# Kernel optimization log

Measured on AMD Instinct MI355X. Metric: run time of the kernel, lower is better.

The kernel has to match this reference:

```python
import jax, jax.numpy as jnp
import numpy as np

DIM = 512
NUM_HEADS = 16
HEAD_DIM = DIM // NUM_HEADS
SCALE = HEAD_DIM ** -0.5  # qk_scale default


def setup_inputs() -> dict:
    key = jax.random.key(0)
    k1, k2, k3 = jax.random.split(key, 3)
    B, nH, nW, C = 8, 256, 49, DIM
    x = jax.random.normal(k1, (B, nH, nW, C), dtype=jnp.float32)
    x_all = jax.random.normal(k2, (B, nH, nW, C), dtype=jnp.float32)
    W_qkv = jax.random.normal(k3, (C, 3 * C), dtype=jnp.float32) * (C ** -0.5)
    b_qkv = jnp.zeros((3 * C,), dtype=jnp.float32)
    return {"x": x, "x_all": x_all, "W_qkv": W_qkv, "b_qkv": b_qkv}


def reference(x, x_all, W_qkv, b_qkv):
    # x: [B, nH, nW, C]  (nH = num windows, nW = tokens per window)
    B, nH, nW, C = x.shape
    qkv = x @ W_qkv + b_qkv                      # [B, nH, nW, 3C]
    qkv = qkv.reshape(B, nH, nW, 3, C)
    q, k, v = qkv[..., 0, :], qkv[..., 1, :], qkv[..., 2, :]
    q = q * SCALE
    attn = jnp.einsum("bwic,bwjc->bwij", q, k)   # [B, nH, nW, nW]
    attn = jax.nn.softmax(attn, axis=-1)
    out = jnp.einsum("bwij,bwjc->bwic", attn, v)  # [B, nH, nW, C]
    return out
```

## Files before the change

kernel.cpp:

```cpp
#include <hip/hip_runtime.h>

typedef __bf16 bf16;
typedef __bf16 bf16x4 __attribute__((ext_vector_type(4)));
typedef __bf16 bf16x8 __attribute__((ext_vector_type(8)));
typedef float f32x16 __attribute__((ext_vector_type(16)));

#define SCALE 0.17677669529663687f

__device__ inline f32x16 fzero16() {
  f32x16 v;
  #pragma unroll
  for (int i = 0; i < 16; ++i) v[i] = 0.f;
  return v;
}

__global__ __launch_bounds__(256) void k_mqk(const float* __restrict__ W, bf16* __restrict__ Mqk) {
  __shared__ float Wkt[32][65];
  __shared__ float Wqt[32][65];
  const int tb = (blockIdx.x >> 4) * 32;
  const int ta = (blockIdx.x & 15) * 32;
  const int tid = threadIdx.x;
  const int a_l = tid & 31, b_l = (tid >> 5) * 4;
  float acc[4] = {0.f, 0.f, 0.f, 0.f};
  for (int c0 = 0; c0 < 512; c0 += 64) {
    __syncthreads();
    for (int i = tid; i < 2048; i += 256) {
      int r = i >> 6, c = i & 63;
      Wkt[r][c] = W[(size_t)(tb + r) * 1536 + 512 + c0 + c];
      Wqt[r][c] = W[(size_t)(ta + r) * 1536 + c0 + c];
    }
    __syncthreads();
    for (int c = 0; c < 64; ++c) {
      float wq = Wqt[a_l][c];
      #pragma unroll
      for (int i = 0; i < 4; ++i) acc[i] += Wkt[b_l + i][c] * wq;
    }
  }
  #pragma unroll
  for (int i = 0; i < 4; ++i)
    Mqk[(size_t)(tb + b_l + i) * 512 + ta + a_l] = (bf16)(SCALE * acc[i]);
}

__global__ __launch_bounds__(256) void k_wvt(const float* __restrict__ W, bf16* __restrict__ WvT) {
  const int cin = blockIdx.x;
  int n = threadIdx.x;
  WvT[(size_t)n * 512 + cin] = (bf16)W[(size_t)cin * 1536 + 1024 + n];
  n += 256;
  WvT[(size_t)n * 512 + cin] = (bf16)W[(size_t)cin * 1536 + 1024 + n];
}

__global__ __launch_bounds__(256) void k_w2(const float* __restrict__ W, const float* __restrict__ bqkv,
                                            float* __restrict__ w2) {
  __shared__ float red[256];
  const int b = blockIdx.x, tid = threadIdx.x;
  float s = W[(size_t)b * 1536 + 512 + tid] * bqkv[tid]
          + W[(size_t)b * 1536 + 512 + 256 + tid] * bqkv[256 + tid];
  red[tid] = s;
  __syncthreads();
  for (int ofs = 128; ofs > 0; ofs >>= 1) {
    if (tid < ofs) red[tid] += red[tid + ofs];
    __syncthreads();
  }
  if (tid == 0) w2[b] = SCALE * red[0];
}

struct SMem {
  bf16 Xs[64][520];
  union { bf16 T1s[64][520]; bf16 Vt[512][72]; } u;
  float Ss[52][65];
  bf16 Ps[64][72];
  float sbias[64];
};

__global__ __launch_bounds__(512, 2) void k_attn(
    const float* __restrict__ x, const float* __restrict__ bqkv,
    const bf16* __restrict__ Mqk, const bf16* __restrict__ WvT,
    const float* __restrict__ w2, float* __restrict__ out) {
  __shared__ SMem sm;
  const int tid = threadIdx.x;
  const int wave = tid >> 6, lane = tid & 63;
  const int lm = lane & 31, hk = lane >> 5;
  const int wid = blockIdx.x;
  const float* xw = x + (size_t)wid * 25088;

  for (int idx = tid; idx < 6272; idx += 512) {
    float4 f = ((const float4*)xw)[idx];
    int row = idx >> 7, c4 = (idx & 127) << 2;
    bf16x4 p;
    p[0] = (bf16)f.x; p[1] = (bf16)f.y; p[2] = (bf16)f.z; p[3] = (bf16)f.w;
    *(bf16x4*)&sm.Xs[row][c4] = p;
  }
  for (int idx = tid; idx < 15 * 130; idx += 512) {
    int r = 49 + idx / 130, c = (idx % 130) * 4;
    bf16x4 z; z[0] = (bf16)0.f; z[1] = (bf16)0.f; z[2] = (bf16)0.f; z[3] = (bf16)0.f;
    *(bf16x4*)&sm.Xs[r][c] = z;
  }
  __syncthreads();

  {
    const int n_base = wave * 64;
    f32x16 a00 = fzero16(), a01 = fzero16(), a10 = fzero16(), a11 = fzero16();
    const bf16* a0p = &sm.Xs[lm][0];
    const bf16* a1p = &sm.Xs[32 + lm][0];
    const bf16* b0g = Mqk + (size_t)(n_base + lm) * 512;
    const bf16* b1g = Mqk + (size_t)(n_base + 32 + lm) * 512;
    #pragma unroll 4
    for (int k0 = 0; k0 < 512; k0 += 16) {
      const int ko = k0 + 8 * hk;
      bf16x8 fa0 = *(const bf16x8*)(a0p + ko);
      bf16x8 fa1 = *(const bf16x8*)(a1p + ko);
      bf16x8 fb0 = *(const bf16x8*)(b0g + ko);
      bf16x8 fb1 = *(const bf16x8*)(b1g + ko);
      a00 = __builtin_amdgcn_mfma_f32_32x32x16_bf16(fa0, fb0, a00, 0, 0, 0);
      a01 = __builtin_amdgcn_mfma_f32_32x32x16_bf16(fa0, fb1, a01, 0, 0, 0);
      a10 = __builtin_amdgcn_mfma_f32_32x32x16_bf16(fa1, fb0, a10, 0, 0, 0);
      a11 = __builtin_amdgcn_mfma_f32_32x32x16_bf16(fa1, fb1, a11, 0, 0, 0);
    }
    #pragma unroll
    for (int reg = 0; reg < 16; ++reg) {
      const int row = (reg & 3) + 8 * (reg >> 2) + 4 * hk;
      sm.u.T1s[row][n_base + lm]           = (bf16)a00[reg];
      sm.u.T1s[row][n_base + 32 + lm]      = (bf16)a01[reg];
      sm.u.T1s[32 + row][n_base + lm]      = (bf16)a10[reg];
      sm.u.T1s[32 + row][n_base + 32 + lm] = (bf16)a11[reg];
    }
  }
  __syncthreads();

  if (wave < 4) {
    const int r = wave & 1, c = wave >> 1;
    f32x16 accS = fzero16();
    const bf16* ap = &sm.u.T1s[32 * r + lm][0];
    const bf16* bp = &sm.Xs[32 * c + lm][0];
    #pragma unroll 4
    for (int k0 = 0; k0 < 512; k0 += 16) {
      const int ko = k0 + 8 * hk;
      bf16x8 fa = *(const bf16x8*)(ap + ko);
      bf16x8 fb = *(const bf16x8*)(bp + ko);
      accS = __builtin_amdgcn_mfma_f32_32x32x16_bf16(fa, fb, accS, 0, 0, 0);
    }
    #pragma unroll
    for (int reg = 0; reg < 16; ++reg) {
      const int row = 32 * r + (reg & 3) + 8 * (reg >> 2) + 4 * hk;
      if (row < 52) sm.Ss[row][32 * c + lm] = accS[reg];
    }
  } else {
    const int t2 = tid - 256;
    const int j = t2 >> 2, part = t2 & 3;
    float s = 0.f;
    for (int cc = part * 128; cc < part * 128 + 128; ++cc)
      s += (float)sm.Xs[j][cc] * w2[cc];
    s += __shfl_xor(s, 1);
    s += __shfl_xor(s, 2);
    if (part == 0) sm.sbias[j] = s;
  }
  __syncthreads();

  if (tid < 49) {
    const int i = tid;
    float m = -1e30f;
    for (int j = 0; j < 49; ++j) m = fmaxf(m, sm.Ss[i][j] + sm.sbias[j]);
    float ssum = 0.f;
    for (int j = 0; j < 49; ++j) ssum += __expf(sm.Ss[i][j] + sm.sbias[j] - m);
    const float inv = 1.f / ssum;
    for (int j = 0; j < 49; ++j)
      sm.Ps[i][j] = (bf16)(__expf(sm.Ss[i][j] + sm.sbias[j] - m) * inv);
    for (int j = 49; j < 64; ++j) sm.Ps[i][j] = (bf16)0.f;
  }

  {
    const int n_base = wave * 64;
    f32x16 a00 = fzero16(), a01 = fzero16(), a10 = fzero16(), a11 = fzero16();
    const bf16* a0p = &sm.Xs[lm][0];
    const bf16* a1p = &sm.Xs[32 + lm][0];
    const bf16* b0g = WvT + (size_t)(n_base + lm) * 512;
    const bf16* b1g = WvT + (size_t)(n_base + 32 + lm) * 512;
    #pragma unroll 4
    for (int k0 = 0; k0 < 512; k0 += 16) {
      const int ko = k0 + 8 * hk;
      bf16x8 fa0 = *(const bf16x8*)(a0p + ko);
      bf16x8 fa1 = *(const bf16x8*)(a1p + ko);
      bf16x8 fb0 = *(const bf16x8*)(b0g + ko);
      bf16x8 fb1 = *(const bf16x8*)(b1g + ko);
      a00 = __builtin_amdgcn_mfma_f32_32x32x16_bf16(fa0, fb0, a00, 0, 0, 0);
      a01 = __builtin_amdgcn_mfma_f32_32x32x16_bf16(fa0, fb1, a01, 0, 0, 0);
      a10 = __builtin_amdgcn_mfma_f32_32x32x16_bf16(fa1, fb0, a10, 0, 0, 0);
      a11 = __builtin_amdgcn_mfma_f32_32x32x16_bf16(fa1, fb1, a11, 0, 0, 0);
    }
    const float bv0 = bqkv[1024 + n_base + lm];
    const float bv1 = bqkv[1024 + n_base + 32 + lm];
    #pragma unroll
    for (int g = 0; g < 4; ++g) {
      const int t0 = 8 * g + 4 * hk;
      bf16x4 p0, p1, p2, p3;
      #pragma unroll
      for (int j = 0; j < 4; ++j) {
        p0[j] = (bf16)(a00[4 * g + j] + bv0);
        p1[j] = (bf16)(a01[4 * g + j] + bv1);
        p2[j] = (bf16)(a10[4 * g + j] + bv0);
        p3[j] = (bf16)(a11[4 * g + j] + bv1);
      }
      *(bf16x4*)&sm.u.Vt[n_base + lm][t0]           = p0;
      *(bf16x4*)&sm.u.Vt[n_base + 32 + lm][t0]      = p1;
      *(bf16x4*)&sm.u.Vt[n_base + lm][32 + t0]      = p2;
      *(bf16x4*)&sm.u.Vt[n_base + 32 + lm][32 + t0] = p3;
    }
  }
  __syncthreads();

  {
    const int n_base = wave * 64;
    f32x16 a00 = fzero16(), a01 = fzero16(), a10 = fzero16(), a11 = fzero16();
    #pragma unroll
    for (int k0 = 0; k0 < 64; k0 += 16) {
      const int ko = k0 + 8 * hk;
      bf16x8 fa0 = *(const bf16x8*)&sm.Ps[lm][ko];
      bf16x8 fa1 = *(const bf16x8*)&sm.Ps[32 + lm][ko];
      bf16x8 fb0 = *(const bf16x8*)&sm.u.Vt[n_base + lm][ko];
      bf16x8 fb1 = *(const bf16x8*)&sm.u.Vt[n_base + 32 + lm][ko];
      a00 = __builtin_amdgcn_mfma_f32_32x32x16_bf16(fa0, fb0, a00, 0, 0, 0);
      a01 = __builtin_amdgcn_mfma_f32_32x32x16_bf16(fa0, fb1, a01, 0, 0, 0);
      a10 = __builtin_amdgcn_mfma_f32_32x32x16_bf16(fa1, fb0, a10, 0, 0, 0);
      a11 = __builtin_amdgcn_mfma_f32_32x32x16_bf16(fa1, fb1, a11, 0, 0, 0);
    }
    float* ow = out + (size_t)wid * 25088;
    const int c0_ = n_base + lm, c1_ = n_base + 32 + lm;
    #pragma unroll
    for (int reg = 0; reg < 16; ++reg) {
      const int row = (reg & 3) + 8 * (reg >> 2) + 4 * hk;
      if (row < 49) {
        ow[row * 512 + c0_] = a00[reg];
        ow[row * 512 + c1_] = a01[reg];
      }
      const int row1 = 32 + row;
      if (row1 < 49) {
        ow[row1 * 512 + c0_] = a10[reg];
        ow[row1 * 512 + c1_] = a11[reg];
      }
    }
  }
}

extern "C" void kernel_launch(void* const* d_in, const int* in_sizes, int n_in,
                              void* d_out, int out_size, void* d_ws, size_t ws_size,
                              hipStream_t stream) {
  const float* x    = (const float*)d_in[0];
  const float* W    = (const float*)d_in[2];
  const float* bqkv = (const float*)d_in[3];
  float* out = (float*)d_out;

  bf16*  Mqk = (bf16*)d_ws;
  bf16*  WvT = (bf16*)((char*)d_ws + 512 * 512 * 2);
  float* w2  = (float*)((char*)d_ws + 2 * 512 * 512 * 2);

  k_mqk<<<256, 256, 0, stream>>>(W, Mqk);
  k_wvt<<<512, 256, 0, stream>>>(W, WvT);
  k_w2 <<<512, 256, 0, stream>>>(W, bqkv, w2);
  k_attn<<<2048, 512, 0, stream>>>(x, bqkv, Mqk, WvT, w2, out);
}
```

Measured before the change: 768.7 us.

## Keep attention intermediates in registers, shrink LDS, raise occupancy to four blocks

Computes T1 transposed (Mqk·X^T) so each wave's accumulators can be repacked into MFMA operand fragments with cross-lane shuffles. QK scores are then accumulated across waves into LDS with atomicAdd, and V stays in registers for the PV product. This removes the T1s/Vt LDS buffers, padding-row zeroing and several barriers, which shrinks LDS enough to allow launch_bounds(512,4). The cost is extra register pressure, LDS atomics on the score matrix, and duplicated row-48 loads for the padded tail.

```diff
diff --git a/kernel.cpp b/kernel.cpp
--- a/kernel.cpp
+++ b/kernel.cpp
@@ -1,17 +1,45 @@
 #include <hip/hip_runtime.h>
+#include <stdint.h>
 
 typedef __bf16 bf16;
+typedef __bf16 bf16x2 __attribute__((ext_vector_type(2)));
 typedef __bf16 bf16x4 __attribute__((ext_vector_type(4)));
 typedef __bf16 bf16x8 __attribute__((ext_vector_type(8)));
 typedef float f32x16 __attribute__((ext_vector_type(16)));
 
 #define SCALE 0.17677669529663687f
-
-__device__ inline f32x16 fzero16() {
+#define MFMA32(a, b, c) __builtin_amdgcn_mfma_f32_32x32x16_bf16((a), (b), (c), 0, 0, 0)
+
+__device__ __forceinline__ f32x16 fzero16() {
   f32x16 v;
   #pragma unroll
   for (int i = 0; i < 16; ++i) v[i] = 0.f;
   return v;
+}
+
+__device__ __forceinline__ uint32_t pk2(float a, float b) {
+  union { bf16x2 h; uint32_t u; } c;
+  c.h[0] = (bf16)a; c.h[1] = (bf16)b;
+  return c.u;
+}
+
+template<int HALF>
+__device__ __forceinline__ bf16x8 repack_frag(f32x16 cc, int hk) {
+  const int R = 8 * HALF;
+  uint32_t pA0 = pk2(cc[R + 0], cc[R + 1]);
+  uint32_t pA1 = pk2(cc[R + 2], cc[R + 3]);
+  uint32_t pB0 = pk2(cc[R + 4], cc[R + 5]);
+  uint32_t pB1 = pk2(cc[R + 6], cc[R + 7]);
+  uint32_t sA0 = __shfl_xor(pA0, 32, 64);
+  uint32_t sA1 = __shfl_xor(pA1, 32, 64);
+  uint32_t sB0 = __shfl_xor(pB0, 32, 64);
+  uint32_t sB1 = __shfl_xor(pB1, 32, 64);
+  union { uint32_t u[4]; bf16x8 v; } o;
+  o.u[0] = hk ? sB0 : pA0;
+  o.u[1] = hk ? sB1 : pA1;
+  o.u[2] = hk ? pB0 : sA0;
+  o.u[3] = hk ? pB1 : sA1;
+  return o.v;
 }
 
 __global__ __launch_bounds__(256) void k_mqk(const float* __restrict__ W, bf16* __restrict__ Mqk) {
@@ -64,22 +92,24 @@
   if (tid == 0) w2[b] = SCALE * red[0];
 }
 
-struct SMem {
-  bf16 Xs[64][520];
-  union { bf16 T1s[64][520]; bf16 Vt[512][72]; } u;
-  float Ss[52][65];
-  bf16 Ps[64][72];
+struct __align__(16) SMem {
+  bf16  Xs[49][520];
+  bf16  Ps[64][72];
+  float Ss[49][65];
+  float ws2[512];
   float sbias[64];
 };
 
-__global__ __launch_bounds__(512, 2) void k_attn(
+__global__ __launch_bounds__(512, 4) void k_attn(
     const float* __restrict__ x, const float* __restrict__ bqkv,
     const bf16* __restrict__ Mqk, const bf16* __restrict__ WvT,
     const float* __restrict__ w2, float* __restrict__ out) {
   __shared__ SMem sm;
   const int tid = threadIdx.x;
-  const int wave = tid >> 6, lane = tid & 63;
+  const int lane = tid & 63;
   const int lm = lane & 31, hk = lane >> 5;
+  const int wave = tid >> 6;
+  const int n_base = wave * 64;
   const int wid = blockIdx.x;
   const float* xw = x + (size_t)wid * 25088;
 
@@ -90,153 +120,197 @@
     p[0] = (bf16)f.x; p[1] = (bf16)f.y; p[2] = (bf16)f.z; p[3] = (bf16)f.w;
     *(bf16x4*)&sm.Xs[row][c4] = p;
   }
-  for (int idx = tid; idx < 15 * 130; idx += 512) {
-    int r = 49 + idx / 130, c = (idx % 130) * 4;
-    bf16x4 z; z[0] = (bf16)0.f; z[1] = (bf16)0.f; z[2] = (bf16)0.f; z[3] = (bf16)0.f;
-    *(bf16x4*)&sm.Xs[r][c] = z;
-  }
+  sm.ws2[tid] = w2[tid];
+  for (int i = tid; i < 49 * 65; i += 512) ((float*)&sm.Ss[0][0])[i] = 0.f;
   __syncthreads();
 
-  {
-    const int n_base = wave * 64;
-    f32x16 a00 = fzero16(), a01 = fzero16(), a10 = fzero16(), a11 = fzero16();
-    const bf16* a0p = &sm.Xs[lm][0];
-    const bf16* a1p = &sm.Xs[32 + lm][0];
-    const bf16* b0g = Mqk + (size_t)(n_base + lm) * 512;
-    const bf16* b1g = Mqk + (size_t)(n_base + 32 + lm) * 512;
+  const bf16* xs_lo = &sm.Xs[lm][0];
+  const bf16* xs_hi = &sm.Xs[(32 + lm) < 49 ? (32 + lm) : 48][0];
+
+  f32x16 c100 = fzero16(), c101 = fzero16(), c110 = fzero16(), c111 = fzero16();
+  {
+    const bf16* mq0 = Mqk + (size_t)(n_base + lm) * 512;
+    const bf16* mq1 = Mqk + (size_t)(n_base + 32 + lm) * 512;
     #pragma unroll 4
     for (int k0 = 0; k0 < 512; k0 += 16) {
       const int ko = k0 + 8 * hk;
-      bf16x8 fa0 = *(const bf16x8*)(a0p + ko);
-      bf16x8 fa1 = *(const bf16x8*)(a1p + ko);
-      bf16x8 fb0 = *(const bf16x8*)(b0g + ko);
-      bf16x8 fb1 = *(const bf16x8*)(b1g + ko);
-      a00 = __builtin_amdgcn_mfma_f32_32x32x16_bf16(fa0, fb0, a00, 0, 0, 0);
-      a01 = __builtin_amdgcn_mfma_f32_32x32x16_bf16(fa0, fb1, a01, 0, 0, 0);
-      a10 = __builtin_amdgcn_mfma_f32_32x32x16_bf16(fa1, fb0, a10, 0, 0, 0);
-      a11 = __builtin_amdgcn_mfma_f32_32x32x16_bf16(fa1, fb1, a11, 0, 0, 0);
+      bf16x8 fa0 = *(const bf16x8*)(mq0 + ko);
+      bf16x8 fa1 = *(const bf16x8*)(mq1 + ko);
+      bf16x8 fb0 = *(const bf16x8*)(xs_lo + ko);
+      bf16x8 fb1 = *(const bf16x8*)(xs_hi + ko);
+      c100 = MFMA32(fa0, fb0, c100); c101 = MFMA32(fa0, fb1, c101);
+      c110 = MFMA32(fa1, fb0, c110); c111 = MFMA32(fa1, fb1, c111);
+    }
+  }
+
+  bf16x8 aT0s0 = repack_frag<0>(c100, hk);
+  bf16x8 aT0s1 = repack_frag<1>(c100, hk);
+  bf16x8 aT0s2 = repack_frag<0>(c110, hk);
+  bf16x8 aT0s3 = repack_frag<1>(c110, hk);
+  bf16x8 aT1s0 = repack_frag<0>(c101, hk);
+  bf16x8 aT1s1 = repack_frag<1>(c101, hk);
+  bf16x8 aT1s2 = repack_frag<0>(c111, hk);
+  bf16x8 aT1s3 = repack_frag<1>(c111, hk);
+
+  {
+    f32x16 s00 = fzero16(), s01 = fzero16(), s10 = fzero16(), s11 = fzero16();
+    const bf16* xb0 = xs_lo + n_base;
+    const bf16* xb1 = xs_hi + n_base;
+    const int ho = 8 * hk;
+    {
+      bf16x8 fb0 = *(const bf16x8*)(xb0 + ho +  0);
+      bf16x8 fb1 = *(const bf16x8*)(xb1 + ho +  0);
+      s00 = MFMA32(aT0s0, fb0, s00); s01 = MFMA32(aT0s0, fb1, s01);
+      s10 = MFMA32(aT1s0, fb0, s10); s11 = MFMA32(aT1s0, fb1, s11);
+    }
+    {
+      bf16x8 fb0 = *(const bf16x8*)(xb0 + ho + 16);
+      bf16x8 fb1 = *(const bf16x8*)(xb1 + ho + 16);
+      s00 = MFMA32(aT0s1, fb0, s00); s01 = MFMA32(aT0s1, fb1, s01);
+      s10 = MFMA32(aT1s1, fb0, s10); s11 = MFMA32(aT1s1, fb1, s11);
+    }
+    {
+      bf16x8 fb0 = *(const bf16x8*)(xb0 + ho + 32);
+      bf16x8 fb1 = *(const bf16x8*)(xb1 + ho + 32);
+      s00 = MFMA32(aT0s2, fb0, s00); s01 = MFMA32(aT0s2, fb1, s01);
+      s10 = MFMA32(aT1s2, fb0, s10); s11 = MFMA32(aT1s2, fb1, s11);
+    }
+    {
+      bf16x8 fb0 = *(const bf16x8*)(xb0 + ho + 48);
+      bf16x8 fb1 = *(const bf16x8*)(xb1 + ho + 48);
+      s00 = MFMA32(aT0s3, fb0, s00); s01 = MFMA32(aT0s3, fb1, s01);
+      s10 = MFMA32(aT1s3, fb0, s10); s11 = MFMA32(aT1s3, fb1, s11);
     }
     #pragma unroll
-    for (int reg = 0; reg < 16; ++reg) {
-      const int row = (reg & 3) + 8 * (reg >> 2) + 4 * hk;
-      sm.u.T1s[row][n_base + lm]           = (bf16)a00[reg];
-      sm.u.T1s[row][n_base + 32 + lm]      = (bf16)a01[reg];
-      sm.u.T1s[32 + row][n_base + lm]      = (bf16)a10[reg];
-      sm.u.T1s[32 + row][n_base + 32 + lm] = (bf16)a11[reg];
-    }
-  }
-  __syncthreads();
-
-  if (wave < 4) {
-    const int r = wave & 1, c = wave >> 1;
-    f32x16 accS = fzero16();
-    const bf16* ap = &sm.u.T1s[32 * r + lm][0];
-    const bf16* bp = &sm.Xs[32 * c + lm][0];
+    for (int r = 0; r < 16; ++r) {
+      const int row = (r & 3) + 8 * (r >> 2) + 4 * hk;
+      if (row < 49) {
+        atomicAdd(&sm.Ss[row][lm],      s00[r]);
+        atomicAdd(&sm.Ss[row][32 + lm], s01[r]);
+      }
+      const int row1 = 32 + row;
+      if (row1 < 49) {
+        atomicAdd(&sm.Ss[row1][lm],      s10[r]);
+        atomicAdd(&sm.Ss[row1][32 + lm], s11[r]);
+      }
+    }
+  }
+
+  {
+    const int brow = tid >> 3, bsub = tid & 7;
+    if (brow < 49) {
+      const bf16* xr = &sm.Xs[brow][bsub * 64];
+      const float* wr = &sm.ws2[bsub * 64];
+      float s = 0.f;
+      #pragma unroll
+      for (int t = 0; t < 8; ++t) {
+        bf16x8 xv = *(const bf16x8*)(xr + 8 * t);
+        #pragma unroll
+        for (int e = 0; e < 8; ++e) s += (float)xv[e] * wr[8 * t + e];
+      }
+      s += __shfl_xor(s, 1, 64);
+      s += __shfl_xor(s, 2, 64);
+      s += __shfl_xor(s, 4, 64);
+      if (bsub == 0) sm.sbias[brow] = s;
+    }
+  }
+
+  f32x16 v00 = fzero16(), v01 = fzero16(), v10 = fzero16(), v11 = fzero16();
+  {
+    const bf16* wv0 = WvT + (size_t)(n_base + lm) * 512;
+    const bf16* wv1 = WvT + (size_t)(n_base + 32 + lm) * 512;
     #pragma unroll 4
     for (int k0 = 0; k0 < 512; k0 += 16) {
       const int ko = k0 + 8 * hk;
-      bf16x8 fa = *(const bf16x8*)(ap + ko);
-      bf16x8 fb = *(const bf16x8*)(bp + ko);
-      accS = __builtin_amdgcn_mfma_f32_32x32x16_bf16(fa, fb, accS, 0, 0, 0);
-    }
-    #pragma unroll
-    for (int reg = 0; reg < 16; ++reg) {
-      const int row = 32 * r + (reg & 3) + 8 * (reg >> 2) + 4 * hk;
-      if (row < 52) sm.Ss[row][32 * c + lm] = accS[reg];
-    }
-  } else {
-    const int t2 = tid - 256;
-    const int j = t2 >> 2, part = t2 & 3;
-    float s = 0.f;
-    for (int cc = part * 128; cc < part * 128 + 128; ++cc)
-      s += (float)sm.Xs[j][cc] * w2[cc];
-    s += __shfl_xor(s, 1);
-    s += __shfl_xor(s, 2);
-    if (part == 0) sm.sbias[j] = s;
-  }
-  __syncthreads();
-
-  if (tid < 49) {
-    const int i = tid;
-    float m = -1e30f;
-    for (int j = 0; j < 49; ++j) m = fmaxf(m, sm.Ss[i][j] + sm.sbias[j]);
-    float ssum = 0.f;
-    for (int j = 0; j < 49; ++j) ssum += __expf(sm.Ss[i][j] + sm.sbias[j] - m);
-    const float inv = 1.f / ssum;
-    for (int j = 0; j < 49; ++j)
-      sm.Ps[i][j] = (bf16)(__expf(sm.Ss[i][j] + sm.sbias[j] - m) * inv);
-    for (int j = 49; j < 64; ++j) sm.Ps[i][j] = (bf16)0.f;
-  }
-
-  {
-    const int n_base = wave * 64;
-    f32x16 a00 = fzero16(), a01 = fzero16(), a10 = fzero16(), a11 = fzero16();
-    const bf16* a0p = &sm.Xs[lm][0];
-    const bf16* a1p = &sm.Xs[32 + lm][0];
-    const bf16* b0g = WvT + (size_t)(n_base + lm) * 512;
-    const bf16* b1g = WvT + (size_t)(n_base + 32 + lm) * 512;
-    #pragma unroll 4
-    for (int k0 = 0; k0 < 512; k0 += 16) {
-      const int ko = k0 + 8 * hk;
-      bf16x8 fa0 = *(const bf16x8*)(a0p + ko);
-      bf16x8 fa1 = *(const bf16x8*)(a1p + ko);
-      bf16x8 fb0 = *(const bf16x8*)(b0g + ko);
-      bf16x8 fb1 = *(const bf16x8*)(b1g + ko);
-      a00 = __builtin_amdgcn_mfma_f32_32x32x16_bf16(fa0, fb0, a00, 0, 0, 0);
-      a01 = __builtin_amdgcn_mfma_f32_32x32x16_bf16(fa0, fb1, a01, 0, 0, 0);
-      a10 = __builtin_amdgcn_mfma_f32_32x32x16_bf16(fa1, fb0, a10, 0, 0, 0);
-      a11 = __builtin_amdgcn_mfma_f32_32x32x16_bf16(fa1, fb1, a11, 0, 0, 0);
+      bf16x8 fa0 = *(const bf16x8*)(xs_lo + ko);
+      bf16x8 fa1 = *(const bf16x8*)(xs_hi + ko);
+      bf16x8 fb0 = *(const bf16x8*)(wv0 + ko);
+      bf16x8 fb1 = *(const bf16x8*)(wv1 + ko);
+      v00 = MFMA32(fa0, fb0, v00); v01 = MFMA32(fa0, fb1, v01);
+      v10 = MFMA32(fa1, fb0, v10); v11 = MFMA32(fa1, fb1, v11);
     }
     const float bv0 = bqkv[1024 + n_base + lm];
     const float bv1 = bqkv[1024 + n_base + 32 + lm];
     #pragma unroll
-    for (int g = 0; g < 4; ++g) {
-      const int t0 = 8 * g + 4 * hk;
-      bf16x4 p0, p1, p2, p3;
-      #pragma unroll
-      for (int j = 0; j < 4; ++j) {
-        p0[j] = (bf16)(a00[4 * g + j] + bv0);
-        p1[j] = (bf16)(a01[4 * g + j] + bv1);
-        p2[j] = (bf16)(a10[4 * g + j] + bv0);
-        p3[j] = (bf16)(a11[4 * g + j] + bv1);
-      }
-      *(bf16x4*)&sm.u.Vt[n_base + lm][t0]           = p0;
-      *(bf16x4*)&sm.u.Vt[n_base + 32 + lm][t0]      = p1;
-      *(bf16x4*)&sm.u.Vt[n_base + lm][32 + t0]      = p2;
-      *(bf16x4*)&sm.u.Vt[n_base + 32 + lm][32 + t0] = p3;
-    }
-  }
+    for (int r = 0; r < 16; ++r) {
+      v00[r] += bv0; v01[r] += bv1; v10[r] += bv0; v11[r] += bv1;
+    }
+  }
+  bf16x8 bV00 = repack_frag<0>(v00, hk);
+  bf16x8 bV01 = repack_frag<1>(v00, hk);
+  bf16x8 bV02 = repack_frag<0>(v10, hk);
+  bf16x8 bV03 = repack_frag<1>(v10, hk);
+  bf16x8 bV10 = repack_frag<0>(v01, hk);
+  bf16x8 bV11 = repack_frag<1>(v01, hk);
+  bf16x8 bV12 = repack_frag<0>(v11, hk);
+  bf16x8 bV13 = repack_frag<1>(v11, hk);
+
   __syncthreads();
 
   {
-    const int n_base = wave * 64;
-    f32x16 a00 = fzero16(), a01 = fzero16(), a10 = fzero16(), a11 = fzero16();
-    #pragma unroll
-    for (int k0 = 0; k0 < 64; k0 += 16) {
-      const int ko = k0 + 8 * hk;
-      bf16x8 fa0 = *(const bf16x8*)&sm.Ps[lm][ko];
-      bf16x8 fa1 = *(const bf16x8*)&sm.Ps[32 + lm][ko];
-      bf16x8 fb0 = *(const bf16x8*)&sm.u.Vt[n_base + lm][ko];
-      bf16x8 fb1 = *(const bf16x8*)&sm.u.Vt[n_base + 32 + lm][ko];
-      a00 = __builtin_amdgcn_mfma_f32_32x32x16_bf16(fa0, fb0, a00, 0, 0, 0);
-      a01 = __builtin_amdgcn_mfma_f32_32x32x16_bf16(fa0, fb1, a01, 0, 0, 0);
-      a10 = __builtin_amdgcn_mfma_f32_32x32x16_bf16(fa1, fb0, a10, 0, 0, 0);
-      a11 = __builtin_amdgcn_mfma_f32_32x32x16_bf16(fa1, fb1, a11, 0, 0, 0);
-    }
-    float* ow = out + (size_t)wid * 25088;
-    const int c0_ = n_base + lm, c1_ = n_base + 32 + lm;
-    #pragma unroll
-    for (int reg = 0; reg < 16; ++reg) {
-      const int row = (reg & 3) + 8 * (reg >> 2) + 4 * hk;
-      if (row < 49) {
-        ow[row * 512 + c0_] = a00[reg];
-        ow[row * 512 + c1_] = a01[reg];
-      }
-      const int row1 = 32 + row;
-      if (row1 < 49) {
-        ow[row1 * 512 + c0_] = a10[reg];
-        ow[row1 * 512 + c1_] = a11[reg];
-      }
+    const int srow = tid >> 3, sub = tid & 7;
+    if (srow < 49) {
+      float v[8];
+      #pragma unroll
+      for (int t = 0; t < 8; ++t) {
+        const int col = sub + 8 * t;
+        v[t] = (col < 49) ? (sm.Ss[srow][col] + sm.sbias[col]) : -1e30f;
+      }
+      float m = v[0];
+      #pragma unroll
+      for (int t = 1; t < 8; ++t) m = fmaxf(m, v[t]);
+      m = fmaxf(m, __shfl_xor(m, 1, 64));
+      m = fmaxf(m, __shfl_xor(m, 2, 64));
+      m = fmaxf(m, __shfl_xor(m, 4, 64));
+      float e[8]; float ssum = 0.f;
+      #pragma unroll
+      for (int t = 0; t < 8; ++t) {
+        const int col = sub + 8 * t;
+        e[t] = (col < 49) ? __expf(v[t] - m) : 0.f;
+        ssum += e[t];
+      }
+      ssum += __shfl_xor(ssum, 1, 64);
+      ssum += __shfl_xor(ssum, 2, 64);
+      ssum += __shfl_xor(ssum, 4, 64);
+      const float inv = 1.f / ssum;
+      #pragma unroll
+      for (int t = 0; t < 8; ++t)
+        sm.Ps[srow][sub + 8 * t] = (bf16)(e[t] * inv);
+    }
+  }
+  __syncthreads();
+
+  f32x16 o00 = fzero16(), o01 = fzero16(), o10 = fzero16(), o11 = fzero16();
+  {
+    const bf16* p0 = &sm.Ps[lm][8 * hk];
+    const bf16* p1 = &sm.Ps[32 + lm][8 * hk];
+    bf16x8 fa0, fa1;
+    fa0 = *(const bf16x8*)(p0 +  0); fa1 = *(const bf16x8*)(p1 +  0);
+    o00 = MFMA32(fa0, bV00, o00); o01 = MFMA32(fa0, bV10, o01);
+    o10 = MFMA32(fa1, bV00, o10); o11 = MFMA32(fa1, bV10, o11);
+    fa0 = *(const bf16x8*)(p0 + 16); fa1 = *(const bf16x8*)(p1 + 16);
+    o00 = MFMA32(fa0, bV01, o00); o01 = MFMA32(fa0, bV11, o01);
+    o10 = MFMA32(fa1, bV01, o10); o11 = MFMA32(fa1, bV11, o11);
+    fa0 = *(const bf16x8*)(p0 + 32); fa1 = *(const bf16x8*)(p1 + 32);
+    o00 = MFMA32(fa0, bV02, o00); o01 = MFMA32(fa0, bV12, o01);
+    o10 = MFMA32(fa1, bV02, o10); o11 = MFMA32(fa1, bV12, o11);
+    fa0 = *(const bf16x8*)(p0 + 48); fa1 = *(const bf16x8*)(p1 + 48);
+    o00 = MFMA32(fa0, bV03, o00); o01 = MFMA32(fa0, bV13, o01);
+    o10 = MFMA32(fa1, bV03, o10); o11 = MFMA32(fa1, bV13, o11);
+  }
+  float* ow = out + (size_t)wid * 25088;
+  const int c0_ = n_base + lm, c1_ = n_base + 32 + lm;
+  #pragma unroll
+  for (int r = 0; r < 16; ++r) {
+    const int row = (r & 3) + 8 * (r >> 2) + 4 * hk;
+    if (row < 49) {
+      ow[row * 512 + c0_] = o00[r];
+      ow[row * 512 + c1_] = o01[r];
+    }
+    const int row1 = 32 + row;
+    if (row1 < 49) {
+      ow[row1 * 512 + c0_] = o10[r];
+      ow[row1 * 512 + c1_] = o11[r];
     }
   }
 }
```

New measurement: 916.9 us. 19.3% more time.

## Fuse V projection into first GEMM loop, parallelize softmax, tile WvT transpose

Applied to the files above, without the earlier changes.

The V projection GEMM is merged into the X·Mqk loop, so each loaded X fragment feeds eight MFMAs and the X shared-memory reads are shared. The V accumulators stay in registers across the score and softmax phases. Softmax now uses 8 threads per row with shuffle reductions instead of one serial thread per row. The WvT transpose kernel now goes through a shared-memory tile with coalesced vector accesses. Holding 128 extra accumulator registers through the middle phases may raise register pressure or cause spills and lower occupancy.

```diff
diff --git a/kernel.cpp b/kernel.cpp
--- a/kernel.cpp
+++ b/kernel.cpp
@@ -1,4 +1,5 @@
 #include <hip/hip_runtime.h>
+#include <stdint.h>
 
 typedef __bf16 bf16;
 typedef __bf16 bf16x4 __attribute__((ext_vector_type(4)));
@@ -6,8 +7,9 @@
 typedef float f32x16 __attribute__((ext_vector_type(16)));
 
 #define SCALE 0.17677669529663687f
-
-__device__ inline f32x16 fzero16() {
+#define MFMA32(a, b, c) __builtin_amdgcn_mfma_f32_32x32x16_bf16((a), (b), (c), 0, 0, 0)
+
+__device__ __forceinline__ f32x16 fzero16() {
   f32x16 v;
   #pragma unroll
   for (int i = 0; i < 16; ++i) v[i] = 0.f;
@@ -42,11 +44,32 @@
 }
 
 __global__ __launch_bounds__(256) void k_wvt(const float* __restrict__ W, bf16* __restrict__ WvT) {
-  const int cin = blockIdx.x;
-  int n = threadIdx.x;
-  WvT[(size_t)n * 512 + cin] = (bf16)W[(size_t)cin * 1536 + 1024 + n];
-  n += 256;
-  WvT[(size_t)n * 512 + cin] = (bf16)W[(size_t)cin * 1536 + 1024 + n];
+  __shared__ float Wt[64][68];
+  const int cin0  = (blockIdx.x & 7) * 64;
+  const int cout0 = (blockIdx.x >> 3) * 64;
+  const int tid = threadIdx.x;
+  {
+    const int r = tid >> 2, cq = (tid & 3) * 16;
+    #pragma unroll
+    for (int cc = 0; cc < 4; ++cc) {
+      float4 f = *(const float4*)&W[(size_t)(cin0 + r) * 1536 + 1024 + cout0 + cq + 4 * cc];
+      Wt[r][cq + 4 * cc + 0] = f.x;
+      Wt[r][cq + 4 * cc + 1] = f.y;
+      Wt[r][cq + 4 * cc + 2] = f.z;
+      Wt[r][cq + 4 * cc + 3] = f.w;
+    }
+  }
+  __syncthreads();
+  {
+    const int co = tid >> 2, seg = (tid & 3) * 16;
+    bf16x8 p0, p1;
+    #pragma unroll
+    for (int e = 0; e < 8; ++e) p0[e] = (bf16)Wt[seg + e][co];
+    #pragma unroll
+    for (int e = 0; e < 8; ++e) p1[e] = (bf16)Wt[seg + 8 + e][co];
+    *(bf16x8*)&WvT[(size_t)(cout0 + co) * 512 + cin0 + seg]     = p0;
+    *(bf16x8*)&WvT[(size_t)(cout0 + co) * 512 + cin0 + seg + 8] = p1;
+  }
 }
 
 __global__ __launch_bounds__(256) void k_w2(const float* __restrict__ W, const float* __restrict__ bqkv,
@@ -97,32 +120,38 @@
   }
   __syncthreads();
 
+  f32x16 v00, v01, v10, v11;
   {
     const int n_base = wave * 64;
-    f32x16 a00 = fzero16(), a01 = fzero16(), a10 = fzero16(), a11 = fzero16();
+    f32x16 t00 = fzero16(), t01 = fzero16(), t10 = fzero16(), t11 = fzero16();
+    v00 = fzero16(); v01 = fzero16(); v10 = fzero16(); v11 = fzero16();
     const bf16* a0p = &sm.Xs[lm][0];
     const bf16* a1p = &sm.Xs[32 + lm][0];
     const bf16* b0g = Mqk + (size_t)(n_base + lm) * 512;
     const bf16* b1g = Mqk + (size_t)(n_base + 32 + lm) * 512;
-    #pragma unroll 4
+    const bf16* c0g = WvT + (size_t)(n_base + lm) * 512;
+    const bf16* c1g = WvT + (size_t)(n_base + 32 + lm) * 512;
+    #pragma unroll 2
     for (int k0 = 0; k0 < 512; k0 += 16) {
       const int ko = k0 + 8 * hk;
       bf16x8 fa0 = *(const bf16x8*)(a0p + ko);
       bf16x8 fa1 = *(const bf16x8*)(a1p + ko);
       bf16x8 fb0 = *(const bf16x8*)(b0g + ko);
       bf16x8 fb1 = *(const bf16x8*)(b1g + ko);
-      a00 = __builtin_amdgcn_mfma_f32_32x32x16_bf16(fa0, fb0, a00, 0, 0, 0);
-      a01 = __builtin_amdgcn_mfma_f32_32x32x16_bf16(fa0, fb1, a01, 0, 0, 0);
-      a10 = __builtin_amdgcn_mfma_f32_32x32x16_bf16(fa1, fb0, a10, 0, 0, 0);
-      a11 = __builtin_amdgcn_mfma_f32_32x32x16_bf16(fa1, fb1, a11, 0, 0, 0);
+      bf16x8 fc0 = *(const bf16x8*)(c0g + ko);
+      bf16x8 fc1 = *(const bf16x8*)(c1g + ko);
+      t00 = MFMA32(fa0, fb0, t00); t01 = MFMA32(fa0, fb1, t01);
+      t10 = MFMA32(fa1, fb0, t10); t11 = MFMA32(fa1, fb1, t11);
+      v00 = MFMA32(fa0, fc0, v00); v01 = MFMA32(fa0, fc1, v01);
+      v10 = MFMA32(fa1, fc0, v10); v11 = MFMA32(fa1, fc1, v11);
     }
     #pragma unroll
     for (int reg = 0; reg < 16; ++reg) {
       const int row = (reg & 3) + 8 * (reg >> 2) + 4 * hk;
-      sm.u.T1s[row][n_base + lm]           = (bf16)a00[reg];
-      sm.u.T1s[row][n_base + 32 + lm]      = (bf16)a01[reg];
-      sm.u.T1s[32 + row][n_base + lm]      = (bf16)a10[reg];
-      sm.u.T1s[32 + row][n_base + 32 + lm] = (bf16)a11[reg];
+      sm.u.T1s[row][n_base + lm]           = (bf16)t00[reg];
+      sm.u.T1s[row][n_base + 32 + lm]      = (bf16)t01[reg];
+      sm.u.T1s[32 + row][n_base + lm]      = (bf16)t10[reg];
+      sm.u.T1s[32 + row][n_base + 32 + lm] = (bf16)t11[reg];
     }
   }
   __syncthreads();
@@ -137,7 +166,7 @@
       const int ko = k0 + 8 * hk;
       bf16x8 fa = *(const bf16x8*)(ap + ko);
       bf16x8 fb = *(const bf16x8*)(bp + ko);
-      accS = __builtin_amdgcn_mfma_f32_32x32x16_bf16(fa, fb, accS, 0, 0, 0);
+      accS = MFMA32(fa, fb, accS);
     }
     #pragma unroll
     for (int reg = 0; reg < 16; ++reg) {
@@ -156,37 +185,40 @@
   }
   __syncthreads();
 
-  if (tid < 49) {
-    const int i = tid;
-    float m = -1e30f;
-    for (int j = 0; j < 49; ++j) m = fmaxf(m, sm.Ss[i][j] + sm.sbias[j]);
-    float ssum = 0.f;
-    for (int j = 0; j < 49; ++j) ssum += __expf(sm.Ss[i][j] + sm.sbias[j] - m);
-    const float inv = 1.f / ssum;
-    for (int j = 0; j < 49; ++j)
-      sm.Ps[i][j] = (bf16)(__expf(sm.Ss[i][j] + sm.sbias[j] - m) * inv);
-    for (int j = 49; j < 64; ++j) sm.Ps[i][j] = (bf16)0.f;
+  {
+    const int srow = tid >> 3, sub = tid & 7;
+    if (srow < 49) {
+      float v[8];
+      #pragma unroll
+      for (int t = 0; t < 8; ++t) {
+        const int col = sub + 8 * t;
+        v[t] = (col < 49) ? (sm.Ss[srow][col] + sm.sbias[col]) : -1e30f;
+      }
+      float m = v[0];
+      #pragma unroll
+      for (int t = 1; t < 8; ++t) m = fmaxf(m, v[t]);
+      m = fmaxf(m, __shfl_xor(m, 1, 64));
+      m = fmaxf(m, __shfl_xor(m, 2, 64));
+      m = fmaxf(m, __shfl_xor(m, 4, 64));
+      float e[8]; float ssum = 0.f;
+      #pragma unroll
+      for (int t = 0; t < 8; ++t) {
+        const int col = sub + 8 * t;
+        e[t] = (col < 49) ? __expf(v[t] - m) : 0.f;
+        ssum += e[t];
+      }
+      ssum += __shfl_xor(ssum, 1, 64);
+      ssum += __shfl_xor(ssum, 2, 64);
+      ssum += __shfl_xor(ssum, 4, 64);
+      const float inv = 1.f / ssum;
+      #pragma unroll
+      for (int t = 0; t < 8; ++t)
+        sm.Ps[srow][sub + 8 * t] = (bf16)(e[t] * inv);
+    }
   }
 
   {
     const int n_base = wave * 64;
-    f32x16 a00 = fzero16(), a01 = fzero16(), a10 = fzero16(), a11 = fzero16();
-    const bf16* a0p = &sm.Xs[lm][0];
-    const bf16* a1p = &sm.Xs[32 + lm][0];
-    const bf16* b0g = WvT + (size_t)(n_base + lm) * 512;
-    const bf16* b1g = WvT + (size_t)(n_base + 32 + lm) * 512;
-    #pragma unroll 4
-    for (int k0 = 0; k0 < 512; k0 += 16) {
-      const int ko = k0 + 8 * hk;
-      bf16x8 fa0 = *(const bf16x8*)(a0p + ko);
-      bf16x8 fa1 = *(const bf16x8*)(a1p + ko);
-      bf16x8 fb0 = *(const bf16x8*)(b0g + ko);
-      bf16x8 fb1 = *(const bf16x8*)(b1g + ko);
-      a00 = __builtin_amdgcn_mfma_f32_32x32x16_bf16(fa0, fb0, a00, 0, 0, 0);
-      a01 = __builtin_amdgcn_mfma_f32_32x32x16_bf16(fa0, fb1, a01, 0, 0, 0);
-      a10 = __builtin_amdgcn_mfma_f32_32x32x16_bf16(fa1, fb0, a10, 0, 0, 0);
-      a11 = __builtin_amdgcn_mfma_f32_32x32x16_bf16(fa1, fb1, a11, 0, 0, 0);
-    }
     const float bv0 = bqkv[1024 + n_base + lm];
     const float bv1 = bqkv[1024 + n_base + 32 + lm];
     #pragma unroll
@@ -195,10 +227,10 @@
       bf16x4 p0, p1, p2, p3;
       #pragma unroll
       for (int j = 0; j < 4; ++j) {
-        p0[j] = (bf16)(a00[4 * g + j] + bv0);
-        p1[j] = (bf16)(a01[4 * g + j] + bv1);
-        p2[j] = (bf16)(a10[4 * g + j] + bv0);
-        p3[j] = (bf16)(a11[4 * g + j] + bv1);
+        p0[j] = (bf16)(v00[4 * g + j] + bv0);
+        p1[j] = (bf16)(v01[4 * g + j] + bv1);
+        p2[j] = (bf16)(v10[4 * g + j] + bv0);
+        p3[j] = (bf16)(v11[4 * g + j] + bv1);
       }
       *(bf16x4*)&sm.u.Vt[n_base + lm][t0]           = p0;
       *(bf16x4*)&sm.u.Vt[n_base + 32 + lm][t0]      = p1;
@@ -218,10 +250,8 @@
       bf16x8 fa1 = *(const bf16x8*)&sm.Ps[32 + lm][ko];
       bf16x8 fb0 = *(const bf16x8*)&sm.u.Vt[n_base + lm][ko];
       bf16x8 fb1 = *(const bf16x8*)&sm.u.Vt[n_base + 32 + lm][ko];
-      a00 = __builtin_amdgcn_mfma_f32_32x32x16_bf16(fa0, fb0, a00, 0, 0, 0);
-      a01 = __builtin_amdgcn_mfma_f32_32x32x16_bf16(fa0, fb1, a01, 0, 0, 0);
-      a10 = __builtin_amdgcn_mfma_f32_32x32x16_bf16(fa1, fb0, a10, 0, 0, 0);
-      a11 = __builtin_amdgcn_mfma_f32_32x32x16_bf16(fa1, fb1, a11, 0, 0, 0);
+      a00 = MFMA32(fa0, fb0, a00); a01 = MFMA32(fa0, fb1, a01);
+      a10 = MFMA32(fa1, fb0, a10); a11 = MFMA32(fa1, fb1, a11);
     }
     float* ow = out + (size_t)wid * 25088;
     const int c0_ = n_base + lm, c1_ = n_base + 32 + lm;
@@ -254,7 +284,7 @@
   float* w2  = (float*)((char*)d_ws + 2 * 512 * 512 * 2);
 
   k_mqk<<<256, 256, 0, stream>>>(W, Mqk);
-  k_wvt<<<512, 256, 0, stream>>>(W, WvT);
+  k_wvt<<<64, 256, 0, stream>>>(W, WvT);
   k_w2 <<<512, 256, 0, stream>>>(W, bqkv, w2);
   k_attn<<<2048, 512, 0, stream>>>(x, bqkv, Mqk, WvT, w2, out);
 }
```

Result: no change. 773.3 us (+0.6%).
